# Performance work log

Measured on AMD Instinct MI355X. Metric: run time of the kernel, lower is better.

## Reference

```python
import jax, jax.numpy as jnp
import numpy as np

NUM_HEADS = 8
LN_EPS = 1e-5


def _layernorm(x, g, b):
    m = jnp.mean(x, axis=-1, keepdims=True)
    v = jnp.mean(jnp.square(x - m), axis=-1, keepdims=True)
    return (x - m) * jax.lax.rsqrt(v + LN_EPS) * g + b


def setup_inputs() -> dict:
    key = jax.random.key(0)
    ks = jax.random.split(key, 10)
    D, C, Cin = 2, 256, 64  # depth, embed dim, input channels
    w = lambda k, shape: jax.random.normal(k, shape, jnp.float32) * 0.02
    return {
        "x": jax.random.normal(ks[0], (4, Cin, 12, 12, 12), jnp.float32),
        "W_pe": w(ks[1], (Cin, C)),
        "b_pe": jnp.zeros((C,), jnp.float32),
        "cls_token": w(ks[2], (1, 1, C)),
        "ln1_g": jnp.ones((D, C), jnp.float32),
        "ln1_b": jnp.zeros((D, C), jnp.float32),
        "Wqkv": w(ks[3], (D, C, 3 * C)),
        "Wproj": w(ks[4], (D, C, C)),
        "bproj": jnp.zeros((D, C), jnp.float32),
        "ln2_g": jnp.ones((D, C), jnp.float32),
        "ln2_b": jnp.zeros((D, C), jnp.float32),
        "W1": w(ks[5], (D, C, C)),
        "b1": jnp.zeros((D, C), jnp.float32),
        "W2": w(ks[6], (D, C, C)),
        "b2": jnp.zeros((D, C), jnp.float32),
        "normf_g": jnp.ones((C,), jnp.float32),
        "normf_b": jnp.zeros((C,), jnp.float32),
    }


def reference(x, W_pe, b_pe, cls_token, ln1_g, ln1_b, Wqkv, Wproj, bproj,
              ln2_g, ln2_b, W1, b1, W2, b2, normf_g, normf_b):
    B, Cin, H, W, L = x.shape
    C = W_pe.shape[1]
    hd = C // NUM_HEADS
    scale = hd ** (-0.5)

    # PatchEmbed: 1x1x1 Conv3d == per-voxel linear projection, then flatten to tokens
    tok = jnp.einsum('bchwl,cd->bhwld', x, W_pe).reshape(B, H * W * L, C) + b_pe
    cls = jnp.broadcast_to(cls_token, (B, 1, C))
    t = jnp.concatenate([cls, tok], axis=1)  # [B, N, C], N = H*W*L + 1
    N = t.shape[1]

    depth = Wqkv.shape[0]
    for i in range(depth):
        # --- self-attention ---
        y = _layernorm(t, ln1_g[i], ln1_b[i])
        qkv = (y @ Wqkv[i]).reshape(B, N, 3, NUM_HEADS, hd)
        qkv = jnp.transpose(qkv, (2, 0, 3, 1, 4))  # [3, B, H, N, hd]
        q, k, v = qkv[0], qkv[1], qkv[2]
        attn = jnp.einsum('bhnd,bhmd->bhnm', q, k) * scale
        attn = jax.nn.softmax(attn, axis=-1)
        o = jnp.einsum('bhnm,bhmd->bhnd', attn, v)
        o = jnp.transpose(o, (0, 2, 1, 3)).reshape(B, N, C)
        t = t + (o @ Wproj[i] + bproj[i])
        # --- MLP (mlp_ratio=1.0, exact GELU) ---
        y = _layernorm(t, ln2_g[i], ln2_b[i])
        h = jax.nn.gelu(y @ W1[i] + b1[i], approximate=False)
        t = t + (h @ W2[i] + b2[i])

    t = _layernorm(t, normf_g, normf_b)
    x_cls = t[:, 0]                                   # [B, C]
    feat = t[:, 1:]                                   # [B, H*W*L, C]
    feat = jnp.transpose(feat, (0, 2, 1)).reshape(B, C, H, W, L)  # downsample = Identity for dim=256
    return x_cls, feat
```

## Files before the change

kernel.cpp:

```cpp
#include <hip/hip_runtime.h>
#include <hip/hip_bf16.h>
#include <math.h>

#define B_   4
#define CIN  64
#define P_   1728
#define N_   1729
#define C_   256
#define NH_  8
#define HD_  32
#define M_   (B_*N_)
#define NPAD 1792

typedef __bf16 bf16x8 __attribute__((ext_vector_type(8)));
typedef __bf16 bf16x4 __attribute__((ext_vector_type(4)));
typedef float  f32x4  __attribute__((ext_vector_type(4)));

__global__ __launch_bounds__(256) void embed2(
    const float* __restrict__ x, const float* __restrict__ Wpe,
    const float* __restrict__ bpe, const float* __restrict__ cls,
    float* __restrict__ t)
{
    int idx = blockIdx.x*256 + threadIdx.x;
    int c   = idx & 255;
    int n   = (idx >> 8) % N_;
    int b   = idx / (N_*256);
    if (n == 0) { t[idx] = cls[c]; return; }
    int p = n - 1;
    float acc = bpe[c];
    for (int ci = 0; ci < CIN; ++ci)
        acc += x[(size_t)(b*CIN + ci)*P_ + p] * Wpe[ci*C_ + c];
    t[idx] = acc;
}

__global__ __launch_bounds__(256) void ln4(
    const float* __restrict__ in, __bf16* __restrict__ out,
    const float* __restrict__ g, const float* __restrict__ bb)
{
    int wv = threadIdx.x >> 6, lane = threadIdx.x & 63;
    size_t row = (size_t)blockIdx.x*4 + wv;
    float4 v = *(const float4*)&in[row*C_ + lane*4];
    float s1 = (v.x+v.y)+(v.z+v.w);
    float s2 = (v.x*v.x+v.y*v.y)+(v.z*v.z+v.w*v.w);
    #pragma unroll
    for (int off = 32; off >= 1; off >>= 1) {
        s1 += __shfl_xor(s1, off);
        s2 += __shfl_xor(s2, off);
    }
    float mean = s1*(1.0f/C_);
    float var  = fmaxf(s2*(1.0f/C_) - mean*mean, 0.0f);
    float rstd = rsqrtf(var + 1e-5f);
    float4 gg = *(const float4*)&g[lane*4];
    float4 bv = *(const float4*)&bb[lane*4];
    bf16x4 r;
    r[0] = (__bf16)((v.x-mean)*rstd*gg.x + bv.x);
    r[1] = (__bf16)((v.y-mean)*rstd*gg.y + bv.y);
    r[2] = (__bf16)((v.z-mean)*rstd*gg.z + bv.z);
    r[3] = (__bf16)((v.w-mean)*rstd*gg.w + bv.w);
    *(bf16x4*)&out[row*C_ + lane*4] = r;
}

__global__ __launch_bounds__(256) void ln4f(
    const float* __restrict__ in, float* __restrict__ out,
    const float* __restrict__ g, const float* __restrict__ bb,
    float* __restrict__ cls_out)
{
    int wv = threadIdx.x >> 6, lane = threadIdx.x & 63;
    size_t row = (size_t)blockIdx.x*4 + wv;
    float4 v = *(const float4*)&in[row*C_ + lane*4];
    float s1 = (v.x+v.y)+(v.z+v.w);
    float s2 = (v.x*v.x+v.y*v.y)+(v.z*v.z+v.w*v.w);
    #pragma unroll
    for (int off = 32; off >= 1; off >>= 1) {
        s1 += __shfl_xor(s1, off);
        s2 += __shfl_xor(s2, off);
    }
    float mean = s1*(1.0f/C_);
    float var  = fmaxf(s2*(1.0f/C_) - mean*mean, 0.0f);
    float rstd = rsqrtf(var + 1e-5f);
    float4 gg = *(const float4*)&g[lane*4];
    float4 bv = *(const float4*)&bb[lane*4];
    float4 r;
    r.x = (v.x-mean)*rstd*gg.x + bv.x;
    r.y = (v.y-mean)*rstd*gg.y + bv.y;
    r.z = (v.z-mean)*rstd*gg.z + bv.z;
    r.w = (v.w-mean)*rstd*gg.w + bv.w;
    *(float4*)&out[row*C_ + lane*4] = r;
    if ((row % N_) == 0)
        *(float4*)&cls_out[(row / N_)*C_ + lane*4] = r;
}

__global__ __launch_bounds__(256) void wprep2(
    const float* __restrict__ Wqkv, const float* __restrict__ Wproj,
    const float* __restrict__ W1,   const float* __restrict__ W2,
    __bf16* __restrict__ wT)
{
    int z = blockIdx.z, which = z >> 1, layer = z & 1;
    const float* src; __bf16* dst; int NC;
    if (which == 0) {
        src = Wqkv + (size_t)layer*C_*768;
        dst = wT   + (size_t)layer*768*256;
        NC  = 768;
    } else {
        NC = 256;
        const float* b3 = (which == 1) ? Wproj : (which == 2) ? W1 : W2;
        src = b3 + (size_t)layer*65536;
        dst = wT + 2*768*256 + (size_t)((which-1)*2 + layer)*65536;
    }
    int n0 = blockIdx.x*32; if (n0 >= NC) return;
    int k0 = blockIdx.y*32;
    __shared__ float tile[32][33];
    int c = threadIdx.x & 31, r = threadIdx.x >> 5;
    for (int rr = r; rr < 32; rr += 8)
        tile[rr][c] = src[(size_t)(k0+rr)*NC + n0 + c];
    __syncthreads();
    for (int rr = r; rr < 32; rr += 8)
        dst[(size_t)(n0+rr)*256 + k0 + c] = (__bf16)tile[c][rr];
}

__global__ __launch_bounds__(256) void padzero(
    __bf16* __restrict__ kB, __bf16* __restrict__ vB)
{
    int idx = blockIdx.x*256 + threadIdx.x;
    if (idx >= 32*63*32) return;
    int d  = idx & 31;
    int n  = (idx >> 5) % 63 + N_;
    int bh = idx / (63*32);
    kB[((size_t)bh*NPAD + n)*32 + d] = (__bf16)0.f;
    vB[((size_t)bh*32 + d)*NPAD + n] = (__bf16)0.f;
}

template<int NC, bool ADD, bool GELU, bool BIAS, bool OUTBF>
__global__ __launch_bounds__(256) void gemm3(
    const __bf16* __restrict__ A, const __bf16* __restrict__ Wt,
    const float* __restrict__ bias, float* __restrict__ outF,
    __bf16* __restrict__ outB)
{
    __shared__ __align__(16) __bf16 As[64*64];
    __shared__ __align__(16) __bf16 Bs[64*64];
    int r0 = blockIdx.x*64, c0 = blockIdx.y*64;
    int tid = threadIdx.x;
    int wv = tid >> 6, lane = tid & 63, quad = lane >> 4, mn = lane & 15;
    int sr = tid >> 2, sc = tid & 3;
    int ga = r0 + sr; if (ga >= M_) ga = M_ - 1;

    f32x4 acc[4];
    #pragma unroll
    for (int ct = 0; ct < 4; ++ct)
        #pragma unroll
        for (int rr = 0; rr < 4; ++rr) acc[ct][rr] = 0.f;

    for (int kc = 0; kc < 4; ++kc) {
        __syncthreads();
        *(bf16x8*)&As[sr*64 + ((sc ^ (sr & 7))*8)] =
            *(const bf16x8*)&A[(size_t)ga*256 + kc*64 + sc*8];
        *(bf16x8*)&As[sr*64 + (((sc+4) ^ (sr & 7))*8)] =
            *(const bf16x8*)&A[(size_t)ga*256 + kc*64 + sc*8 + 32];
        *(bf16x8*)&Bs[sr*64 + ((sc ^ (sr & 7))*8)] =
            *(const bf16x8*)&Wt[(size_t)(c0+sr)*256 + kc*64 + sc*8];
        *(bf16x8*)&Bs[sr*64 + (((sc+4) ^ (sr & 7))*8)] =
            *(const bf16x8*)&Wt[(size_t)(c0+sr)*256 + kc*64 + sc*8 + 32];
        __syncthreads();

        #pragma unroll
        for (int h = 0; h < 2; ++h) {
            bf16x8 a = *(const bf16x8*)&As[(wv*16 + mn)*64 + (((h*4+quad) ^ (mn & 7))*8)];
            #pragma unroll
            for (int ct = 0; ct < 4; ++ct) {
                bf16x8 b = *(const bf16x8*)&Bs[(ct*16 + mn)*64 + (((h*4+quad) ^ (mn & 7))*8)];
                acc[ct] = __builtin_amdgcn_mfma_f32_16x16x32_bf16(a, b, acc[ct], 0, 0, 0);
            }
        }
    }

    #pragma unroll
    for (int ct = 0; ct < 4; ++ct) {
        int col = c0 + ct*16 + mn;
        #pragma unroll
        for (int rr = 0; rr < 4; ++rr) {
            int row = r0 + wv*16 + quad*4 + rr;
            if (row >= M_) continue;
            float val = acc[ct][rr];
            if (BIAS) val += bias[col];
            if (GELU) val = 0.5f*val*(1.f + erff(val*0.70710678118654752f));
            size_t oi = (size_t)row*NC + col;
            if (OUTBF) outB[oi] = (__bf16)val;
            else if (ADD) outF[oi] += val;
            else outF[oi] = val;
        }
    }
}

__global__ __launch_bounds__(256) void gemm_qkv3(
    const __bf16* __restrict__ A, const __bf16* __restrict__ Wt,
    __bf16* __restrict__ qB, __bf16* __restrict__ kB, __bf16* __restrict__ vB)
{
    __shared__ __align__(16) __bf16 As[64*64];
    __shared__ __align__(16) __bf16 Bs[64*64];
    int r0 = blockIdx.x*64, c0 = blockIdx.y*64;
    int tid = threadIdx.x;
    int wv = tid >> 6, lane = tid & 63, quad = lane >> 4, mn = lane & 15;
    int sr = tid >> 2, sc = tid & 3;
    int ga = r0 + sr; if (ga >= M_) ga = M_ - 1;

    f32x4 acc[4];
    #pragma unroll
    for (int ct = 0; ct < 4; ++ct)
        #pragma unroll
        for (int rr = 0; rr < 4; ++rr) acc[ct][rr] = 0.f;

    for (int kc = 0; kc < 4; ++kc) {
        __syncthreads();
        *(bf16x8*)&As[sr*64 + ((sc ^ (sr & 7))*8)] =
            *(const bf16x8*)&A[(size_t)ga*256 + kc*64 + sc*8];
        *(bf16x8*)&As[sr*64 + (((sc+4) ^ (sr & 7))*8)] =
            *(const bf16x8*)&A[(size_t)ga*256 + kc*64 + sc*8 + 32];
        *(bf16x8*)&Bs[sr*64 + ((sc ^ (sr & 7))*8)] =
            *(const bf16x8*)&Wt[(size_t)(c0+sr)*256 + kc*64 + sc*8];
        *(bf16x8*)&Bs[sr*64 + (((sc+4) ^ (sr & 7))*8)] =
            *(const bf16x8*)&Wt[(size_t)(c0+sr)*256 + kc*64 + sc*8 + 32];
        __syncthreads();

        #pragma unroll
        for (int h = 0; h < 2; ++h) {
            bf16x8 a = *(const bf16x8*)&As[(wv*16 + mn)*64 + (((h*4+quad) ^ (mn & 7))*8)];
            #pragma unroll
            for (int ct = 0; ct < 4; ++ct) {
                bf16x8 b = *(const bf16x8*)&Bs[(ct*16 + mn)*64 + (((h*4+quad) ^ (mn & 7))*8)];
                acc[ct] = __builtin_amdgcn_mfma_f32_16x16x32_bf16(a, b, acc[ct], 0, 0, 0);
            }
        }
    }

    const float scale = 0.17677669529663687f;
    #pragma unroll
    for (int ct = 0; ct < 4; ++ct) {
        int col = c0 + ct*16 + mn;
        #pragma unroll
        for (int rr = 0; rr < 4; ++rr) {
            int row = r0 + wv*16 + quad*4 + rr;
            if (row >= M_) continue;
            int b = row / N_, n = row - b*N_;
            float val = acc[ct][rr];
            if (col < 256) {
                int h = col >> 5, dd = col & 31;
                qB[((size_t)(b*NH_+h)*NPAD + n)*32 + dd] = (__bf16)(val*scale);
            } else if (col < 512) {
                int h = (col-256) >> 5, dd = col & 31;
                kB[((size_t)(b*NH_+h)*NPAD + n)*32 + dd] = (__bf16)val;
            } else {
                int h = (col-512) >> 5, dd = col & 31;
                vB[((size_t)(b*NH_+h)*32 + dd)*NPAD + n] = (__bf16)val;
            }
        }
    }
}

__global__ __launch_bounds__(256) void attn11(
    const __bf16* __restrict__ qB, const __bf16* __restrict__ kB,
    const __bf16* __restrict__ vB, __bf16* __restrict__ o)
{
    int bh = blockIdx.x, b = bh >> 3, h = bh & 7;
    int q0 = blockIdx.y * 64;
    int tid = threadIdx.x;
    int wv = tid >> 6, lane = tid & 63, quad = lane >> 4, mn = lane & 15;

    __shared__ __align__(16) __bf16 lk[128*32];
    __shared__ __align__(16) __bf16 lvt[32*128];
    __shared__ __align__(16) __bf16 lp[4][16*72];

    bf16x8 qfrag = *(const bf16x8*)(
        qB + ((size_t)bh*NPAD + q0 + wv*16 + mn)*32 + quad*8);

    f32x4 oacc0, oacc1;
    #pragma unroll
    for (int rr = 0; rr < 4; ++rr) { oacc0[rr]=0.f; oacc1[rr]=0.f; }
    float lsum = 0.f;

    const __bf16* kbase = kB + (size_t)bh*NPAD*32;
    const __bf16* vbase = vB + (size_t)bh*32*NPAD;
    int sr = tid >> 2, sc = tid & 3;
    int vr = tid >> 3, vc = tid & 7;

    for (int t = 0; t < 14; ++t) {
        int k0 = t*128;
        __syncthreads();
        #pragma unroll
        for (int hh = 0; hh < 2; ++hh) {
            int r = hh*64 + sr;
            *(bf16x8*)&lk[r*32 + ((sc ^ (r & 3))*8)] =
                *(const bf16x8*)(kbase + (size_t)(k0 + r)*32 + sc*8);
            int cp = hh*8 + vc;
            *(bf16x8*)&lvt[vr*128 + ((cp ^ (vr & 7))*8)] =
                *(const bf16x8*)(vbase + (size_t)vr*NPAD + k0 + cp*8);
        }
        __syncthreads();

        #pragma unroll
        for (int h2 = 0; h2 < 2; ++h2) {
            #pragma unroll
            for (int ct = 0; ct < 4; ++ct) {
                int kr = h2*64 + ct*16 + mn;
                bf16x8 kf = *(const bf16x8*)&lk[kr*32 + ((quad ^ (mn & 3))*8)];
                f32x4 z;
                #pragma unroll
                for (int rr = 0; rr < 4; ++rr) z[rr] = 0.f;
                f32x4 st = __builtin_amdgcn_mfma_f32_16x16x32_bf16(kf, qfrag, z, 0, 0, 0);

                bf16x4 pf4;
                #pragma unroll
                for (int rr = 0; rr < 4; ++rr) {
                    float p = __expf(st[rr]);
                    pf4[rr] = (__bf16)p;
                    lsum += p;
                }
                *(bf16x4*)&lp[wv][mn*72 + ct*16 + quad*4] = pf4;
            }

            #pragma unroll
            for (int kh = 0; kh < 2; ++kh) {
                bf16x8 pf = *(const bf16x8*)&lp[wv][mn*72 + kh*32 + quad*8];
                int chunk = h2*8 + kh*4 + quad;
                int vsw = (chunk ^ (mn & 7)) * 8;
                bf16x8 v0 = *(const bf16x8*)&lvt[ mn      *128 + vsw];
                bf16x8 v1 = *(const bf16x8*)&lvt[(mn+16)*128 + vsw];
                oacc0 = __builtin_amdgcn_mfma_f32_16x16x32_bf16(pf, v0, oacc0, 0, 0, 0);
                oacc1 = __builtin_amdgcn_mfma_f32_16x16x32_bf16(pf, v1, oacc1, 0, 0, 0);
            }
        }
    }

    lsum += __shfl_xor(lsum, 16);
    lsum += __shfl_xor(lsum, 32);
    lsum -= 63.0f;

    #pragma unroll
    for (int rr = 0; rr < 4; ++rr) {
        float l = __shfl(lsum, quad*4 + rr);
        int q = q0 + wv*16 + quad*4 + rr;
        if (q >= N_) continue;
        float inv = 1.0f / l;
        size_t base = ((size_t)(b*N_ + q))*C_ + h*HD_;
        o[base + mn]      = (__bf16)(oacc0[rr]*inv);
        o[base + 16 + mn] = (__bf16)(oacc1[rr]*inv);
    }
}

__global__ __launch_bounds__(256) void feat3(
    const float* __restrict__ y, float* __restrict__ outf)
{
    __shared__ float tl[32][33];
    int p0 = blockIdx.x*32, c0 = blockIdx.y*32, b = blockIdx.z;
    int cc = threadIdx.x & 31, rr = threadIdx.x >> 5;
    for (int i = rr; i < 32; i += 8)
        tl[i][cc] = y[((size_t)(b*N_) + 1 + p0 + i)*C_ + c0 + cc];
    __syncthreads();
    for (int i = rr; i < 32; i += 8)
        outf[((size_t)(b*C_) + c0 + i)*P_ + p0 + cc] = tl[cc][i];
}

extern "C" void kernel_launch(void* const* d_in, const int* in_sizes, int n_in,
                              void* d_out, int out_size, void* d_ws, size_t ws_size,
                              hipStream_t stream)
{
    const float* x        = (const float*)d_in[0];
    const float* W_pe     = (const float*)d_in[1];
    const float* b_pe     = (const float*)d_in[2];
    const float* cls_tok  = (const float*)d_in[3];
    const float* ln1_g    = (const float*)d_in[4];
    const float* ln1_b    = (const float*)d_in[5];
    const float* Wqkv     = (const float*)d_in[6];
    const float* Wproj    = (const float*)d_in[7];
    const float* bproj    = (const float*)d_in[8];
    const float* ln2_g    = (const float*)d_in[9];
    const float* ln2_b    = (const float*)d_in[10];
    const float* W1       = (const float*)d_in[11];
    const float* b1       = (const float*)d_in[12];
    const float* W2       = (const float*)d_in[13];
    const float* b2       = (const float*)d_in[14];
    const float* normf_g  = (const float*)d_in[15];
    const float* normf_b  = (const float*)d_in[16];

    const size_t MC = (size_t)M_*C_;
    float*  ws  = (float*)d_ws;
    float*  t   = ws;
    float*  yf  = ws + MC;
    __bf16* ybf = (__bf16*)(ws + 2*MC);
    __bf16* hbf = (__bf16*)(ws + 2*MC + MC/2);
    __bf16* obf = (__bf16*)(ws + 2*MC + MC);
    __bf16* wT  = (__bf16*)(ws + 2*MC + 3*(MC/2));
    __bf16* qB  = wT + 2*768*256 + 6*256*256;
    __bf16* kB  = qB + (size_t)B_*NH_*NPAD*32;
    __bf16* vB  = kB + (size_t)B_*NH_*NPAD*32;

    __bf16* projT = wT + 2*768*256;
    __bf16* w1T   = projT + 2*256*256;
    __bf16* w2T   = w1T   + 2*256*256;

    float* out_cls  = (float*)d_out;
    float* out_feat = out_cls + B_*C_;

    wprep2<<<dim3(24, 8, 8), 256, 0, stream>>>(Wqkv, Wproj, W1, W2, wT);
    padzero<<<252, 256, 0, stream>>>(kB, vB);
    embed2<<<(B_*N_*C_)/256, 256, 0, stream>>>(x, W_pe, b_pe, cls_tok, t);

    const int GRID_M = (M_ + 63) / 64;
    for (int i = 0; i < 2; ++i) {
        ln4<<<M_/4, 256, 0, stream>>>(t, ybf, ln1_g + i*C_, ln1_b + i*C_);
        gemm_qkv3<<<dim3(GRID_M, 12), 256, 0, stream>>>(
            ybf, wT + (size_t)i*768*256, qB, kB, vB);
        attn11<<<dim3(32, 28), 256, 0, stream>>>(qB, kB, vB, obf);
        gemm3<256,true,false,true,false><<<dim3(GRID_M, 4), 256, 0, stream>>>(
            obf, projT + (size_t)i*65536, bproj + i*C_, t, nullptr);
        ln4<<<M_/4, 256, 0, stream>>>(t, ybf, ln2_g + i*C_, ln2_b + i*C_);
        gemm3<256,false,true,true,true><<<dim3(GRID_M, 4), 256, 0, stream>>>(
            ybf, w1T + (size_t)i*65536, b1 + i*C_, nullptr, hbf);
        gemm3<256,true,false,true,false><<<dim3(GRID_M, 4), 256, 0, stream>>>(
            hbf, w2T + (size_t)i*65536, b2 + i*C_, t, nullptr);
    }

    ln4f<<<M_/4, 256, 0, stream>>>(t, yf, normf_g, normf_b, out_cls);
    feat3<<<dim3(54, 8, 4), 256, 0, stream>>>(yf, out_feat);
}
```

Measured before the change: 296.2 us.

## Rewrite attention with 32x32 MFMA, register P reuse, and prefetched K/V tiles

Replaces the attention kernel with a 128-thread version in which each wave handles 32 query rows using 32x32x16 bf16 MFMAs. The softmax probabilities are packed to bf16 and rearranged across lanes with permlane32 swaps, so they go straight into the PV MFMA without passing through shared memory. The next K/V tile is loaded into registers while the current one is computed, and shared tiles use padded strides in place of XOR swizzles. This adds register pressure and inline asm for gfx950-specific instructions, and halves the threads per block.

```diff
diff --git a/kernel.cpp b/kernel.cpp
--- a/kernel.cpp
+++ b/kernel.cpp
@@ -15,6 +15,7 @@
 typedef __bf16 bf16x8 __attribute__((ext_vector_type(8)));
 typedef __bf16 bf16x4 __attribute__((ext_vector_type(4)));
 typedef float  f32x4  __attribute__((ext_vector_type(4)));
+typedef float  f32x16 __attribute__((ext_vector_type(16)));
 
 __global__ __launch_bounds__(256) void embed2(
     const float* __restrict__ x, const float* __restrict__ Wpe,
@@ -256,93 +257,124 @@
     }
 }
 
-__global__ __launch_bounds__(256) void attn11(
+#define LKS 40
+#define LVS 136
+
+__device__ __forceinline__ unsigned cvtpk_bf16(float lo, float hi) {
+    unsigned r;
+    asm("v_cvt_pk_bf16_f32 %0, %1, %2" : "=v"(r) : "v"(lo), "v"(hi));
+    return r;
+}
+
+__global__ __launch_bounds__(128) void attn12(
     const __bf16* __restrict__ qB, const __bf16* __restrict__ kB,
     const __bf16* __restrict__ vB, __bf16* __restrict__ o)
 {
     int bh = blockIdx.x, b = bh >> 3, h = bh & 7;
     int q0 = blockIdx.y * 64;
     int tid = threadIdx.x;
-    int wv = tid >> 6, lane = tid & 63, quad = lane >> 4, mn = lane & 15;
-
-    __shared__ __align__(16) __bf16 lk[128*32];
-    __shared__ __align__(16) __bf16 lvt[32*128];
-    __shared__ __align__(16) __bf16 lp[4][16*72];
-
-    bf16x8 qfrag = *(const bf16x8*)(
-        qB + ((size_t)bh*NPAD + q0 + wv*16 + mn)*32 + quad*8);
-
-    f32x4 oacc0, oacc1;
-    #pragma unroll
-    for (int rr = 0; rr < 4; ++rr) { oacc0[rr]=0.f; oacc1[rr]=0.f; }
-    float lsum = 0.f;
+    int wv = tid >> 6, lane = tid & 63, lo5 = lane & 31, hi = lane >> 5;
+
+    __shared__ __align__(16) __bf16 lk[128*LKS];
+    __shared__ __align__(16) __bf16 lvt[32*LVS];
 
     const __bf16* kbase = kB + (size_t)bh*NPAD*32;
     const __bf16* vbase = vB + (size_t)bh*32*NPAD;
-    int sr = tid >> 2, sc = tid & 3;
-    int vr = tid >> 3, vc = tid & 7;
+
+    const __bf16* qrow = qB + ((size_t)bh*NPAD + q0 + wv*32 + lo5)*32 + hi*8;
+    bf16x8 qf0 = *(const bf16x8*)(qrow);
+    bf16x8 qf1 = *(const bf16x8*)(qrow + 16);
+
+    f32x16 oacc;
+    #pragma unroll
+    for (int r = 0; r < 16; ++r) oacc[r] = 0.f;
+    float lsum = 0.f;
+
+    int vr = tid >> 2, vc = tid & 3;
+
+    bf16x8 ks0, ks1, ks2, ks3, vs0, vs1, vs2, vs3;
+#define ATTN_LOAD(T) do {                                              \
+        const __bf16* kp_ = kbase + ((size_t)((T)*128 + tid))*32;      \
+        ks0 = *(const bf16x8*)(kp_);                                   \
+        ks1 = *(const bf16x8*)(kp_ + 8);                               \
+        ks2 = *(const bf16x8*)(kp_ + 16);                              \
+        ks3 = *(const bf16x8*)(kp_ + 24);                              \
+        const __bf16* vp_ = vbase + (size_t)vr*NPAD + (T)*128 + vc*32; \
+        vs0 = *(const bf16x8*)(vp_);                                   \
+        vs1 = *(const bf16x8*)(vp_ + 8);                               \
+        vs2 = *(const bf16x8*)(vp_ + 16);                              \
+        vs3 = *(const bf16x8*)(vp_ + 24);                              \
+    } while (0)
+
+    ATTN_LOAD(0);
 
     for (int t = 0; t < 14; ++t) {
-        int k0 = t*128;
-        __syncthreads();
-        #pragma unroll
-        for (int hh = 0; hh < 2; ++hh) {
-            int r = hh*64 + sr;
-            *(bf16x8*)&lk[r*32 + ((sc ^ (r & 3))*8)] =
-                *(const bf16x8*)(kbase + (size_t)(k0 + r)*32 + sc*8);
-            int cp = hh*8 + vc;
-            *(bf16x8*)&lvt[vr*128 + ((cp ^ (vr & 7))*8)] =
-                *(const bf16x8*)(vbase + (size_t)vr*NPAD + k0 + cp*8);
-        }
-        __syncthreads();
-
-        #pragma unroll
-        for (int h2 = 0; h2 < 2; ++h2) {
+        __syncthreads();
+        {
+            __bf16* kd = &lk[tid*LKS];
+            *(bf16x8*)(kd)      = ks0;  *(bf16x8*)(kd + 8)  = ks1;
+            *(bf16x8*)(kd + 16) = ks2;  *(bf16x8*)(kd + 24) = ks3;
+            __bf16* vd = &lvt[vr*LVS + vc*32];
+            *(bf16x8*)(vd)      = vs0;  *(bf16x8*)(vd + 8)  = vs1;
+            *(bf16x8*)(vd + 16) = vs2;  *(bf16x8*)(vd + 24) = vs3;
+        }
+        if (t < 13) ATTN_LOAD(t+1);
+        __syncthreads();
+
+        #pragma unroll
+        for (int kg = 0; kg < 4; ++kg) {
+            const __bf16* kf = &lk[(kg*32 + lo5)*LKS + hi*8];
+            bf16x8 kf0 = *(const bf16x8*)(kf);
+            bf16x8 kf1 = *(const bf16x8*)(kf + 16);
+            f32x16 s;
             #pragma unroll
-            for (int ct = 0; ct < 4; ++ct) {
-                int kr = h2*64 + ct*16 + mn;
-                bf16x8 kf = *(const bf16x8*)&lk[kr*32 + ((quad ^ (mn & 3))*8)];
-                f32x4 z;
-                #pragma unroll
-                for (int rr = 0; rr < 4; ++rr) z[rr] = 0.f;
-                f32x4 st = __builtin_amdgcn_mfma_f32_16x16x32_bf16(kf, qfrag, z, 0, 0, 0);
-
-                bf16x4 pf4;
-                #pragma unroll
-                for (int rr = 0; rr < 4; ++rr) {
-                    float p = __expf(st[rr]);
-                    pf4[rr] = (__bf16)p;
-                    lsum += p;
-                }
-                *(bf16x4*)&lp[wv][mn*72 + ct*16 + quad*4] = pf4;
-            }
-
+            for (int r = 0; r < 16; ++r) s[r] = 0.f;
+            __builtin_amdgcn_s_setprio(1);
+            s = __builtin_amdgcn_mfma_f32_32x32x16_bf16(kf0, qf0, s, 0, 0, 0);
+            s = __builtin_amdgcn_mfma_f32_32x32x16_bf16(kf1, qf1, s, 0, 0, 0);
+            __builtin_amdgcn_s_setprio(0);
+
+            float p[16];
             #pragma unroll
-            for (int kh = 0; kh < 2; ++kh) {
-                bf16x8 pf = *(const bf16x8*)&lp[wv][mn*72 + kh*32 + quad*8];
-                int chunk = h2*8 + kh*4 + quad;
-                int vsw = (chunk ^ (mn & 7)) * 8;
-                bf16x8 v0 = *(const bf16x8*)&lvt[ mn      *128 + vsw];
-                bf16x8 v1 = *(const bf16x8*)&lvt[(mn+16)*128 + vsw];
-                oacc0 = __builtin_amdgcn_mfma_f32_16x16x32_bf16(pf, v0, oacc0, 0, 0, 0);
-                oacc1 = __builtin_amdgcn_mfma_f32_16x16x32_bf16(pf, v1, oacc1, 0, 0, 0);
-            }
-        }
-    }
-
-    lsum += __shfl_xor(lsum, 16);
+            for (int r = 0; r < 16; ++r) p[r] = __expf(s[r]);
+            float l0 = 0.f, l1 = 0.f;
+            #pragma unroll
+            for (int r = 0; r < 8; ++r) { l0 += p[r]; l1 += p[r+8]; }
+            lsum += l0 + l1;
+
+            unsigned a0 = cvtpk_bf16(p[0],  p[1]),  a1 = cvtpk_bf16(p[2],  p[3]);
+            unsigned b0 = cvtpk_bf16(p[4],  p[5]),  b1 = cvtpk_bf16(p[6],  p[7]);
+            unsigned c0 = cvtpk_bf16(p[8],  p[9]),  c1 = cvtpk_bf16(p[10], p[11]);
+            unsigned d0 = cvtpk_bf16(p[12], p[13]), d1 = cvtpk_bf16(p[14], p[15]);
+            asm("v_permlane32_swap_b32 %0, %1" : "+v"(a0), "+v"(b0));
+            asm("v_permlane32_swap_b32 %0, %1" : "+v"(a1), "+v"(b1));
+            asm("v_permlane32_swap_b32 %0, %1" : "+v"(c0), "+v"(d0));
+            asm("v_permlane32_swap_b32 %0, %1" : "+v"(c1), "+v"(d1));
+            union { bf16x8 v; unsigned u[4]; } f0, f1;
+            f0.u[0] = a0; f0.u[1] = a1; f0.u[2] = b0; f0.u[3] = b1;
+            f1.u[0] = c0; f1.u[1] = c1; f1.u[2] = d0; f1.u[3] = d1;
+
+            const __bf16* vf = &lvt[lo5*LVS + kg*32 + hi*8];
+            bf16x8 vf0 = *(const bf16x8*)(vf);
+            bf16x8 vf1 = *(const bf16x8*)(vf + 16);
+            __builtin_amdgcn_s_setprio(1);
+            oacc = __builtin_amdgcn_mfma_f32_32x32x16_bf16(f0.v, vf0, oacc, 0, 0, 0);
+            oacc = __builtin_amdgcn_mfma_f32_32x32x16_bf16(f1.v, vf1, oacc, 0, 0, 0);
+            __builtin_amdgcn_s_setprio(0);
+        }
+    }
+#undef ATTN_LOAD
+
     lsum += __shfl_xor(lsum, 32);
-    lsum -= 63.0f;
-
-    #pragma unroll
-    for (int rr = 0; rr < 4; ++rr) {
-        float l = __shfl(lsum, quad*4 + rr);
-        int q = q0 + wv*16 + quad*4 + rr;
-        if (q >= N_) continue;
-        float inv = 1.0f / l;
-        size_t base = ((size_t)(b*N_ + q))*C_ + h*HD_;
-        o[base + mn]      = (__bf16)(oacc0[rr]*inv);
-        o[base + 16 + mn] = (__bf16)(oacc1[rr]*inv);
+    float inv = 1.0f / (lsum - 63.0f);
+
+    #pragma unroll
+    for (int r = 0; r < 16; ++r) {
+        int qrw = (r & 3) + 8*(r >> 2) + 4*hi;
+        float li = __shfl(inv, qrw);
+        int q = q0 + wv*32 + qrw;
+        if (q < N_)
+            o[((size_t)b*N_ + q)*C_ + h*HD_ + lo5] = (__bf16)(oacc[r] * li);
     }
 }
 
@@ -409,7 +441,7 @@
         ln4<<<M_/4, 256, 0, stream>>>(t, ybf, ln1_g + i*C_, ln1_b + i*C_);
         gemm_qkv3<<<dim3(GRID_M, 12), 256, 0, stream>>>(
             ybf, wT + (size_t)i*768*256, qB, kB, vB);
-        attn11<<<dim3(32, 28), 256, 0, stream>>>(qB, kB, vB, obf);
+        attn12<<<dim3(32, 28), 128, 0, stream>>>(qB, kB, vB, obf);
         gemm3<256,true,false,true,false><<<dim3(GRID_M, 4), 256, 0, stream>>>(
             obf, projT + (size_t)i*65536, bproj + i*C_, t, nullptr);
         ln4<<<M_/4, 256, 0, stream>>>(t, ybf, ln2_g + i*C_, ln2_b + i*C_);
```

Result: faster. 289.5 us (-2.2%).
